# Kernel tuning notes

Hardware: AMD Instinct MI355X
Metric: run time of the kernel (lower is better)

Reference implementation:

```python
import jax, jax.numpy as jnp
import numpy as np


def setup_inputs() -> dict:
    key = jax.random.key(0)
    k1, k2 = jax.random.split(key, 2)
    B, S, H, E = 4, 4096, 4096, 64
    h = jax.random.normal(k1, (B, S, H), dtype=jnp.float32)
    # gate weight as in nn.Linear(hidden_dim, num_experts): W [E, H], bias [E]
    W = jax.random.normal(k2, (E, H), dtype=jnp.float32) * (1.0 / np.sqrt(H))
    b = jnp.zeros((E,), dtype=jnp.float32)
    return {"h": h, "W": W, "b": b, "k": 2}


def reference(h, W, b, k):
    # eval-mode forward (self.training == False, so no gaussian noise)
    # logits: [B, S, E]
    logits = jnp.einsum('bsh,eh->bse', h, W) + b
    E = logits.shape[-1]
    B, S = h.shape[0], h.shape[1]

    # top-k over experts, softmax over the k selected logits
    topk_vals, topk_idx = jax.lax.top_k(logits, k)          # [B, S, k]
    topk_scores = jax.nn.softmax(topk_vals, axis=-1)        # [B, S, k]

    # scatter softmaxed scores back into a zero [B, S, E] tensor
    # (topk indices are distinct, so sum-of-one-hots == scatter)
    route_weights = jnp.sum(
        jax.nn.one_hot(topk_idx, E, dtype=topk_scores.dtype) * topk_scores[..., None],
        axis=-2,
    )  # [B, S, E]

    # aux-loss statistics
    importance = jax.nn.softmax(logits, axis=-1).sum(axis=(0, 1))            # [E]
    load = (route_weights > 0).astype(jnp.float32).sum(axis=(0, 1)) / (B * S)  # [E]
    aux_loss = jnp.mean(importance * load * (E ** 2))
    return route_weights, aux_loss
```

## Files before the change

kernel.cpp:

```cpp
#include <hip/hip_runtime.h>
#include <hip/hip_bf16.h>
#include <math.h>

typedef __attribute__((ext_vector_type(8))) short  short8;
typedef __attribute__((ext_vector_type(4))) float  float4v;

#define NE 64
#define FLAG_CAP 8192
#define EPS_TIE 2e-4f
#define KSPLIT 4

#define BARRIER  asm volatile("s_barrier" ::: "memory")
#define WAITV(n) asm volatile("s_waitcnt vmcnt(" #n ")" ::: "memory")

__device__ __forceinline__ unsigned short f2bf(float x){
  unsigned u = __float_as_uint(x);
  return (unsigned short)((u + 0x7fffu + ((u>>16)&1u)) >> 16);
}
__device__ __forceinline__ float bf2f(unsigned short h){
  return __uint_as_float(((unsigned)h)<<16);
}
__device__ __forceinline__ float warp_sum64(float v){
  #pragma unroll
  for (int off=1; off<64; off<<=1) v += __shfl_xor(v, off, 64);
  return v;
}

__device__ __forceinline__ void gld16(void* lds, const void* g){
  __builtin_amdgcn_global_load_lds(
      (const __attribute__((address_space(1))) unsigned int*)g,
      (__attribute__((address_space(3))) unsigned int*)lds,
      16, 0, 0);
}

__global__ __launch_bounds__(256) void prep_w(
    const float* __restrict__ W, unsigned short* __restrict__ whi,
    unsigned short* __restrict__ wlo, float* __restrict__ zbuf, int K)
{
  if (blockIdx.x == 0){
    #pragma unroll
    for (int i=0;i<5;++i){
      const int idx = threadIdx.x + i*256;
      if (idx < 1025) zbuf[idx] = 0.f;
    }
  }
  const int id = blockIdx.x*256 + threadIdx.x;
  const int nfrag = (K/32)*4*64;
  if (id >= nfrag) return;
  const int lane = id & 63, te = (id>>6)&3, ks = id>>8;
  const int e  = te*16 + (lane&15);
  const int k0 = ks*32 + ((lane>>4)<<3);
  const float* src = W + (size_t)e*K + k0;
  short8 h8, l8;
  #pragma unroll
  for (int j=0;j<8;++j){
    float x = src[j];
    unsigned short hb = f2bf(x);
    h8[j] = (short)hb;
    l8[j] = (short)f2bf(x - bf2f(hb));
  }
  const size_t off = (size_t)id*8;
  *(short8*)(whi + off) = h8;
  *(short8*)(wlo + off) = l8;
}

__device__ __forceinline__ void cvt8b(const float4& c, const float4& d,
                                      short8& hi, short8& lo){
  const float f[8] = {c.x,c.y,c.z,c.w,d.x,d.y,d.z,d.w};
  union { short8 s; unsigned u[4]; } H, L;
  #pragma unroll
  for (int p=0;p<4;++p){
    float2 v = make_float2(f[2*p], f[2*p+1]);
    __hip_bfloat162 hb = __float22bfloat162_rn(v);
    H.u[p] = *reinterpret_cast<unsigned*>(&hb);
    float2 back = __bfloat1622float2(hb);
    float2 res = make_float2(v.x - back.x, v.y - back.y);
    __hip_bfloat162 lb = __float22bfloat162_rn(res);
    L.u[p] = *reinterpret_cast<unsigned*>(&lb);
  }
  hi = H.s; lo = L.s;
}

#define MFMA3(AH, AL, BH, BL, ACC)                                          \
  ACC = __builtin_amdgcn_mfma_f32_16x16x32_bf16(AH, BH, ACC, 0,0,0);        \
  ACC = __builtin_amdgcn_mfma_f32_16x16x32_bf16(AH, BL, ACC, 0,0,0);        \
  ACC = __builtin_amdgcn_mfma_f32_16x16x32_bf16(AL, BH, ACC, 0,0,0);

__global__ __launch_bounds__(256) void gemm_cnt(
    const float* __restrict__ hp, const unsigned short* __restrict__ whi,
    const unsigned short* __restrict__ wlo, float* __restrict__ part,
    int K, long M, int tiles)
{
  __shared__ float          As[2][64*32];
  __shared__ unsigned short Bs[2][8*512];

  const int tid = threadIdx.x;
  const int l = tid & 63, w = tid >> 6;
  const int tok0  = blockIdx.x * 64;
  const int slice = blockIdx.y;
  const int kbase = slice * (tiles*32);
  const int r16 = l & 15, kg = l >> 4;

  float4v acc[4];
  #pragma unroll
  for (int te=0;te<4;++te) acc[te] = (float4v){0.f,0.f,0.f,0.f};

  const unsigned short* bsel[2] = { whi, wlo };
  const int srcblkA = (l&7) ^ (l>>3);

  auto STAGE = [&](int buf, int t){
    #pragma unroll
    for (int i=0;i<2;++i){
      const int row = w*16 + i*8 + (l>>3);
      const float* src = hp + (size_t)(tok0 + row)*K + kbase + t*32 + (srcblkA<<2);
      gld16((void*)(As[buf] + w*512 + i*256), (const void*)src);
    }
    #pragma unroll
    for (int i=0;i<2;++i){
      const int u = w*2 + i;
      const int te = u >> 1, d = u & 1;
      const unsigned short* src = bsel[d]
          + ((size_t)(slice*tiles + t))*2048 + te*512 + (size_t)l*8;
      gld16((void*)(Bs[buf] + u*512), (const void*)src);
    }
  };

  auto COMPUTE = [&](int buf){
    const float* arow = As[buf] + (w*16 + r16)*32;
    const int c0 = kg*2, sw = r16 & 7;
    float4 a0 = *(const float4*)(arow + (((c0  ) ^ sw) << 2));
    float4 a1 = *(const float4*)(arow + (((c0+1) ^ sw) << 2));
    short8 Ah, Al;
    cvt8b(a0, a1, Ah, Al);
    #pragma unroll
    for (int te=0;te<4;++te){
      short8 Bh = *(const short8*)(Bs[buf] + (te*2+0)*512 + l*8);
      short8 Bl = *(const short8*)(Bs[buf] + (te*2+1)*512 + l*8);
      MFMA3(Ah, Al, Bh, Bl, acc[te]);
    }
  };

  STAGE(0, 0);
  STAGE(1, 1);
  WAITV(4); BARRIER;
  int t = 0;
  for (; t < tiles-2; ++t){
    COMPUTE(t&1);
    BARRIER;
    STAGE(t&1, t+2);
    WAITV(4); BARRIER;
  }
  COMPUTE(t&1);
  WAITV(0); BARRIER;
  COMPUTE((t+1)&1);

  float* dst = part + (size_t)slice*M*NE;
  #pragma unroll
  for (int te=0;te<4;++te)
    #pragma unroll
    for (int r=0;r<4;++r){
      const int tok = tok0 + w*16 + (kg<<2) + r;
      dst[(size_t)tok*NE + te*16 + r16] = acc[te][r];
    }
}

__global__ __launch_bounds__(256) void router_finish2(
    const float* __restrict__ part, const float* __restrict__ bp,
    float* __restrict__ outp, float* __restrict__ imp8,
    float* __restrict__ cnt8, int* __restrict__ flagCnt,
    int* __restrict__ flagList, long M)
{
  __shared__ float red[2][4][64];
  const int tid = threadIdx.x;
  const int w = tid >> 6, lane = tid & 63;
  const long base = (long)blockIdx.x*16 + w*4;
  const float bias = bp[lane];
  float impL = 0.f, cntL = 0.f;

  #pragma unroll 1
  for (int it=0; it<4; ++it){
    const long t = base + it;
    float v = part[t*NE + lane];
    v += part[(size_t)M*NE   + t*NE + lane];
    v += part[(size_t)M*NE*2 + t*NE + lane];
    v += part[(size_t)M*NE*3 + t*NE + lane];
    v += bias;
    float m1 = v; int i1 = lane;
    #pragma unroll
    for (int off=1; off<64; off<<=1){
      float ov = __shfl_xor(m1, off, 64);
      int   oi = __shfl_xor(i1, off, 64);
      if (ov > m1 || (ov == m1 && oi < i1)){ m1 = ov; i1 = oi; }
    }
    float vm = (lane == i1) ? -3.4e38f : v;
    float m2 = vm; int i2 = lane;
    #pragma unroll
    for (int off=1; off<64; off<<=1){
      float ov = __shfl_xor(m2, off, 64);
      int   oi = __shfl_xor(i2, off, 64);
      if (ov > m2 || (ov == m2 && oi < i2)){ m2 = ov; i2 = oi; }
    }
    float vm3 = (lane==i1 || lane==i2) ? -3.4e38f : v;
    float m3 = vm3;
    #pragma unroll
    for (int off=1; off<64; off<<=1) m3 = fmaxf(m3, __shfl_xor(m3, off, 64));
    if ((m2 - m3) < EPS_TIE && lane == 0){
      int idx = atomicAdd(flagCnt, 1);
      if (idx < FLAG_CAP) flagList[idx] = (int)t;
    }
    const float ex = __expf(m2 - m1);
    const float s1 = 1.f / (1.f + ex);
    const float s2 = ex * s1;
    const float p = __expf(v - m1);
    const float S = warp_sum64(p);
    impL += p / S;
    const float rw = (lane==i1) ? s1 : ((lane==i2) ? s2 : 0.f);
    outp[t*NE + lane] = rw;
    if (lane==i1 || lane==i2) cntL += 1.f;
  }
  red[0][w][lane] = impL;
  red[1][w][lane] = cntL;
  __syncthreads();
  if (tid < 64){
    float s = red[0][0][tid] + red[0][1][tid] + red[0][2][tid] + red[0][3][tid];
    float c = red[1][0][tid] + red[1][1][tid] + red[1][2][tid] + red[1][3][tid];
    const int g = (blockIdx.x & 7) << 6;
    atomicAdd(&imp8[g + tid], s);
    atomicAdd(&cnt8[g + tid], c);
  }
}

__global__ __launch_bounds__(256) void fixup_aux(
    const float* __restrict__ hp, const float* __restrict__ Wp,
    const float* __restrict__ bp, float* __restrict__ outp,
    const int* __restrict__ flagCnt, const int* __restrict__ flagList,
    const float* __restrict__ imp8, const float* __restrict__ cnt8,
    float* __restrict__ auxp, float scale, int K)
{
  __shared__ float hrow[4096];
  __shared__ float lg[NE];
  if (blockIdx.x == 0 && threadIdx.x < 64){
    float s = 0.f, c = 0.f;
    #pragma unroll
    for (int g=0; g<8; ++g){
      s += imp8[(g<<6) + threadIdx.x];
      c += cnt8[(g<<6) + threadIdx.x];
    }
    float v = s * c;
    v = warp_sum64(v);
    if (threadIdx.x == 0) auxp[0] = v * scale;
  }
  int n = *flagCnt; if (n > FLAG_CAP) n = FLAG_CAP;
  const int e   = threadIdx.x >> 2;
  const int sub = threadIdx.x & 3;
  const int lane = threadIdx.x & 63;

  for (int f = blockIdx.x; f < n; f += gridDim.x){
    const int tok = flagList[f];
    const float* hr = hp + (size_t)tok*K;
    #pragma unroll
    for (int c=0; c<4; ++c){
      const int idx = threadIdx.x*4 + c*1024;
      *(float4*)&hrow[idx] = *(const float4*)(hr + idx);
    }
    __syncthreads();
    const float* wr = Wp + (size_t)e*K;
    float s = 0.f;
    for (int it=0; it<64; ++it){
      const int k0 = it*64 + sub*16;
      #pragma unroll
      for (int u=0; u<4; ++u){
        float4 wv = *(const float4*)(wr + k0 + u*4);
        float4 hv = *(const float4*)(&hrow[k0 + u*4]);
        s = fmaf(hv.x, wv.x, s); s = fmaf(hv.y, wv.y, s);
        s = fmaf(hv.z, wv.z, s); s = fmaf(hv.w, wv.w, s);
      }
    }
    s += __shfl_xor(s, 1, 64);
    s += __shfl_xor(s, 2, 64);
    if (sub == 0) lg[e] = s + bp[e];
    __syncthreads();
    if (threadIdx.x < 64){
      const float v = lg[lane];
      float m1 = v; int i1 = lane;
      #pragma unroll
      for (int off=1; off<64; off<<=1){
        float ov = __shfl_xor(m1, off, 64);
        int   oi = __shfl_xor(i1, off, 64);
        if (ov > m1 || (ov == m1 && oi < i1)){ m1 = ov; i1 = oi; }
      }
      float vm = (lane == i1) ? -3.4e38f : v;
      float m2 = vm; int i2 = lane;
      #pragma unroll
      for (int off=1; off<64; off<<=1){
        float ov = __shfl_xor(m2, off, 64);
        int   oi = __shfl_xor(i2, off, 64);
        if (ov > m2 || (ov == m2 && oi < i2)){ m2 = ov; i2 = oi; }
      }
      const float ex = __expf(m2 - m1);
      const float s1 = 1.f / (1.f + ex);
      const float s2 = ex * s1;
      const float rw = (lane==i1) ? s1 : ((lane==i2) ? s2 : 0.f);
      outp[(size_t)tok * NE + lane] = rw;
    }
    __syncthreads();
  }
}

extern "C" void kernel_launch(void* const* d_in, const int* in_sizes, int n_in,
                              void* d_out, int out_size, void* d_ws, size_t ws_size,
                              hipStream_t stream){
  const float* hp = (const float*)d_in[0];
  const float* Wp = (const float*)d_in[1];
  const float* bp = (const float*)d_in[2];
  const int  E = in_sizes[2];
  const int  K = in_sizes[1] / E;
  const long M = (long)in_sizes[0] / K;

  float* outp = (float*)d_out;
  float* auxp = outp + (size_t)M * E;

  char* ws = (char*)d_ws;
  float* imp8     = (float*)(ws + 0);
  float* cnt8     = (float*)(ws + 2048);
  int*   flagCnt  = (int*)  (ws + 4096);
  int*   flagList = (int*)  (ws + 4160);
  unsigned short* whi = (unsigned short*)(ws + 65536);
  unsigned short* wlo = (unsigned short*)(ws + 65536 + 524288);
  float* part     = (float*)(ws + 1114112);

  const int nfragBlocks = ((K/32)*4*64 + 255)/256;
  const int tiles = (K / KSPLIT) / 32;

  prep_w<<<dim3(nfragBlocks), dim3(256), 0, stream>>>(Wp, whi, wlo, (float*)ws, K);
  gemm_cnt<<<dim3((int)(M/64), KSPLIT), dim3(256), 0, stream>>>(hp, whi, wlo, part, K, M, tiles);
  router_finish2<<<dim3((int)(M/16)), dim3(256), 0, stream>>>(part, bp, outp, imp8, cnt8,
                                                              flagCnt, flagList, M);
  fixup_aux<<<dim3(128), dim3(256), 0, stream>>>(hp, Wp, bp, outp, flagCnt, flagList,
                                                 imp8, cnt8, auxp, (float)E/(float)M, K);
}
```

Baseline: 91.75 us.

## Shrink GEMM token tile to 32 and load weight fragments directly to registers

The gate GEMM now covers 32 tokens per block instead of 64. The four waves split into two token halves times two expert halves. Weight fragments are read straight from global memory into registers, replacing the shared-memory stage, and only the activation tile stays double-buffered in LDS. Launch bounds request 6 blocks per CU. This doubles the grid and cuts LDS use to raise occupancy and latency hiding, but each weight fragment is now fetched by more blocks and each wave issues fewer MFMAs per activation load.

```diff
diff --git a/kernel.cpp b/kernel.cpp
--- a/kernel.cpp
+++ b/kernel.cpp
@@ -86,81 +86,83 @@
   ACC = __builtin_amdgcn_mfma_f32_16x16x32_bf16(AH, BL, ACC, 0,0,0);        \
   ACC = __builtin_amdgcn_mfma_f32_16x16x32_bf16(AL, BH, ACC, 0,0,0);
 
-__global__ __launch_bounds__(256) void gemm_cnt(
+__global__ __launch_bounds__(256, 6) void gemm_cnt(
     const float* __restrict__ hp, const unsigned short* __restrict__ whi,
     const unsigned short* __restrict__ wlo, float* __restrict__ part,
     int K, long M, int tiles)
 {
-  __shared__ float          As[2][64*32];
-  __shared__ unsigned short Bs[2][8*512];
+  __shared__ float As[2][32*32];
 
   const int tid = threadIdx.x;
   const int l = tid & 63, w = tid >> 6;
-  const int tok0  = blockIdx.x * 64;
+  const int tok0  = blockIdx.x * 32;
   const int slice = blockIdx.y;
   const int kbase = slice * (tiles*32);
   const int r16 = l & 15, kg = l >> 4;
-
-  float4v acc[4];
-  #pragma unroll
-  for (int te=0;te<4;++te) acc[te] = (float4v){0.f,0.f,0.f,0.f};
-
-  const unsigned short* bsel[2] = { whi, wlo };
+  const int th = w >> 1, eh = w & 1;
+
+  float4v acc[2];
+  acc[0] = (float4v){0.f,0.f,0.f,0.f};
+  acc[1] = (float4v){0.f,0.f,0.f,0.f};
+
   const int srcblkA = (l&7) ^ (l>>3);
-
-  auto STAGE = [&](int buf, int t){
-    #pragma unroll
-    for (int i=0;i<2;++i){
-      const int row = w*16 + i*8 + (l>>3);
-      const float* src = hp + (size_t)(tok0 + row)*K + kbase + t*32 + (srcblkA<<2);
-      gld16((void*)(As[buf] + w*512 + i*256), (const void*)src);
-    }
-    #pragma unroll
-    for (int i=0;i<2;++i){
-      const int u = w*2 + i;
-      const int te = u >> 1, d = u & 1;
-      const unsigned short* src = bsel[d]
-          + ((size_t)(slice*tiles + t))*2048 + te*512 + (size_t)l*8;
-      gld16((void*)(Bs[buf] + u*512), (const void*)src);
-    }
-  };
-
-  auto COMPUTE = [&](int buf){
-    const float* arow = As[buf] + (w*16 + r16)*32;
-    const int c0 = kg*2, sw = r16 & 7;
-    float4 a0 = *(const float4*)(arow + (((c0  ) ^ sw) << 2));
-    float4 a1 = *(const float4*)(arow + (((c0+1) ^ sw) << 2));
-    short8 Ah, Al;
-    cvt8b(a0, a1, Ah, Al);
-    #pragma unroll
-    for (int te=0;te<4;++te){
-      short8 Bh = *(const short8*)(Bs[buf] + (te*2+0)*512 + l*8);
-      short8 Bl = *(const short8*)(Bs[buf] + (te*2+1)*512 + l*8);
-      MFMA3(Ah, Al, Bh, Bl, acc[te]);
-    }
-  };
-
-  STAGE(0, 0);
-  STAGE(1, 1);
-  WAITV(4); BARRIER;
+  const float* arow_src = hp + (size_t)(tok0 + w*8 + (l>>3))*K + kbase + (srcblkA<<2);
+  const unsigned short* bhp = whi + (size_t)(slice*tiles)*2048 + (eh*2)*512 + (size_t)l*8;
+  const unsigned short* blp = wlo + (size_t)(slice*tiles)*2048 + (eh*2)*512 + (size_t)l*8;
+
+  short8 Bh0, Bl0, Bh1, Bl1;
+
+#define STAGE_A(buf, T) \
+  gld16((void*)(As[buf] + w*256), (const void*)(arow_src + (size_t)(T)*32));
+
+#define LOADB(T) {                                               \
+  const unsigned short* pb = bhp + (size_t)(T)*2048;             \
+  const unsigned short* pl = blp + (size_t)(T)*2048;             \
+  Bh0 = *(const short8*)(pb);                                    \
+  Bl0 = *(const short8*)(pl);                                    \
+  Bh1 = *(const short8*)(pb + 512);                              \
+  Bl1 = *(const short8*)(pl + 512);                              \
+}
+
+#define COMPUTET(buf) {                                          \
+  const float* arow = As[buf] + (th*16 + r16)*32;                \
+  const int c0 = kg*2, sw = r16 & 7;                             \
+  float4 a0 = *(const float4*)(arow + (((c0  ) ^ sw) << 2));     \
+  float4 a1 = *(const float4*)(arow + (((c0+1) ^ sw) << 2));     \
+  short8 Ah, Al;                                                 \
+  cvt8b(a0, a1, Ah, Al);                                         \
+  MFMA3(Ah, Al, Bh0, Bl0, acc[0]);                               \
+  MFMA3(Ah, Al, Bh1, Bl1, acc[1]);                               \
+}
+
+  STAGE_A(0, 0);
+  LOADB(0);
+  STAGE_A(1, 1);
+  WAITV(1); BARRIER;
   int t = 0;
   for (; t < tiles-2; ++t){
-    COMPUTE(t&1);
+    COMPUTET(t&1);
+    LOADB(t+1);
     BARRIER;
-    STAGE(t&1, t+2);
-    WAITV(4); BARRIER;
-  }
-  COMPUTE(t&1);
+    STAGE_A(t&1, t+2);
+    WAITV(1); BARRIER;
+  }
+  COMPUTET(t&1);
+  LOADB(t+1);
   WAITV(0); BARRIER;
-  COMPUTE((t+1)&1);
+  COMPUTET((t+1)&1);
+
+#undef STAGE_A
+#undef LOADB
+#undef COMPUTET
 
   float* dst = part + (size_t)slice*M*NE;
   #pragma unroll
-  for (int te=0;te<4;++te)
+  for (int lt=0;lt<2;++lt)
     #pragma unroll
     for (int r=0;r<4;++r){
-      const int tok = tok0 + w*16 + (kg<<2) + r;
-      dst[(size_t)tok*NE + te*16 + r16] = acc[te][r];
+      const int tok = tok0 + th*16 + (kg<<2) + r;
+      dst[(size_t)tok*NE + (eh*2+lt)*16 + r16] = acc[lt][r];
     }
 }
 
@@ -333,7 +335,7 @@
   const int tiles = (K / KSPLIT) / 32;
 
   prep_w<<<dim3(nfragBlocks), dim3(256), 0, stream>>>(Wp, whi, wlo, (float*)ws, K);
-  gemm_cnt<<<dim3((int)(M/64), KSPLIT), dim3(256), 0, stream>>>(hp, whi, wlo, part, K, M, tiles);
+  gemm_cnt<<<dim3((int)(M/32), KSPLIT), dim3(256), 0, stream>>>(hp, whi, wlo, part, K, M, tiles);
   router_finish2<<<dim3((int)(M/16)), dim3(256), 0, stream>>>(part, bp, outp, imp8, cnt8,
                                                               flagCnt, flagList, M);
   fixup_aux<<<dim3(128), dim3(256), 0, stream>>>(hp, Wp, bp, outp, flagCnt, flagList,
```

After: 114.1 us. 1.24x slower.
